# Performance work log

Measured on AMD Instinct MI355X. Metric: run time of the kernel, lower is better.

The kernel has to match this reference:

```python
import jax, jax.numpy as jnp
import numpy as np

N = 100000   # nodes
E = 1600000  # edges
EL = 200000  # decode pairs
D_IN, D_HID, D_OUT = 128, 128, 64


def setup_inputs() -> dict:
    key = jax.random.key(0)
    ks = jax.random.split(key, 9)
    x = jax.random.normal(ks[0], (N, D_IN), dtype=jnp.float32)
    edge_index = jax.random.randint(ks[1], (2, E), 0, N, dtype=jnp.int64)
    edge_label_index = jax.random.randint(ks[2], (2, EL), 0, N, dtype=jnp.int64)
    # GCNConv params: weight [in, out] (no bias inside linear), bias added after aggregation
    W1 = jax.random.normal(ks[3], (D_IN, D_HID), dtype=jnp.float32) / np.sqrt(D_IN)
    b1 = jnp.zeros((D_HID,), dtype=jnp.float32)
    W2 = jax.random.normal(ks[4], (D_HID, D_HID), dtype=jnp.float32) / np.sqrt(D_HID)
    b2 = jnp.zeros((D_HID,), dtype=jnp.float32)
    W3 = jax.random.normal(ks[5], (D_HID, D_OUT), dtype=jnp.float32) / np.sqrt(D_HID)
    b3 = jnp.zeros((D_OUT,), dtype=jnp.float32)
    return {"x": x, "edge_index": edge_index, "edge_label_index": edge_label_index,
            "W1": W1, "b1": b1, "W2": W2, "b2": b2, "W3": W3, "b3": b3}


def _gcn_norm(edge_index, num_nodes, dtype):
    # add self-loops, compute symmetric normalization deg^-1/2[src]*deg^-1/2[dst]
    loop = jnp.arange(num_nodes, dtype=edge_index.dtype)
    src = jnp.concatenate([edge_index[0], loop])
    dst = jnp.concatenate([edge_index[1], loop])
    deg = jax.ops.segment_sum(jnp.ones(src.shape, dtype=dtype), dst, num_segments=num_nodes)
    dinv = jax.lax.rsqrt(deg)  # deg >= 1 due to self-loops
    norm = dinv[src] * dinv[dst]
    return src, dst, norm


def _gcn_conv(h, W, b, src, dst, norm, num_nodes):
    h = h @ W                               # [N, out]
    msg = h[src] * norm[:, None]            # gather + scale  [E+N, out]
    out = jax.ops.segment_sum(msg, dst, num_segments=num_nodes)  # scatter-add
    return out + b


def reference(x, edge_index, edge_label_index, W1, b1, W2, b2, W3, b3):
    num_nodes = x.shape[0]
    src, dst, norm = _gcn_norm(edge_index, num_nodes, x.dtype)
    h = jax.nn.relu(_gcn_conv(x, W1, b1, src, dst, norm, num_nodes))
    h = jax.nn.relu(_gcn_conv(h, W2, b2, src, dst, norm, num_nodes))  # dropout is identity in eval
    z = _gcn_conv(h, W3, b3, src, dst, norm, num_nodes)
    # decode: dot product over candidate pairs
    return jnp.sum(z[edge_label_index[0]] * z[edge_label_index[1]], axis=-1)
```

## Files before the change

kernel.cpp:

```cpp
#include <hip/hip_runtime.h>
#include <hip/hip_bf16.h>

#define N_NODES 100000
#define N_EDGES 1600000
#define N_EL    200000

#define NB_SCAN ((N_NODES + 255) / 256)
#define CPAD 16
#define GT_GEMM ((N_NODES + 63) / 64)
#define GE_RANK ((N_EDGES + 255) / 256)

typedef unsigned int uint32;
typedef unsigned short ushort16;
typedef __attribute__((ext_vector_type(8))) short short8;
typedef __attribute__((ext_vector_type(4))) float f32x4;

static __device__ __forceinline__ ushort16 f2bf(float f) {
    uint32 u = __float_as_uint(f);
    u += 0x7fffu + ((u >> 16) & 1u);
    return (ushort16)(u >> 16);
}
static __device__ __forceinline__ float bf_lo(uint32 p) { return __uint_as_float(p << 16); }
static __device__ __forceinline__ float bf_hi(uint32 p) { return __uint_as_float(p & 0xffff0000u); }
static __device__ __forceinline__ float bf2f(ushort16 h) { return __uint_as_float((uint32)h << 16); }

__global__ void k_scan1(const int* __restrict__ cpad, int* __restrict__ rowptr,
                        int* __restrict__ bsum, float* __restrict__ dinv) {
    __shared__ int s[256];
    int t = threadIdx.x;
    int i = blockIdx.x * 256 + t;
    int v = (i < N_NODES) ? cpad[(size_t)i * CPAD] : 0;
    if (i < N_NODES) dinv[i] = 1.0f / sqrtf((float)(v + 1));
    s[t] = v;
    __syncthreads();
    for (int off = 1; off < 256; off <<= 1) {
        int u = (t >= off) ? s[t - off] : 0;
        __syncthreads();
        s[t] += u;
        __syncthreads();
    }
    if (i < N_NODES) rowptr[i] = s[t] - v;
    if (t == 255) bsum[blockIdx.x] = s[255];
}

__global__ void k_scan2(const int* __restrict__ bsum, int* __restrict__ boff) {
    __shared__ int s[512];
    int t = threadIdx.x;
    int v = (t < NB_SCAN) ? bsum[t] : 0;
    s[t] = v;
    __syncthreads();
    for (int off = 1; off < 512; off <<= 1) {
        int u = (t >= off) ? s[t - off] : 0;
        __syncthreads();
        s[t] += u;
        __syncthreads();
    }
    if (t < NB_SCAN) boff[t] = s[t] - v;
    if (t == NB_SCAN - 1) boff[NB_SCAN] = s[t];
}

__global__ void k_scan3(int* __restrict__ rowptr, const int* __restrict__ boff) {
    int i = blockIdx.x * 256 + threadIdx.x;
    if (i < N_NODES) rowptr[i] += boff[blockIdx.x];
    if (i == 0) rowptr[N_NODES] = boff[NB_SCAN];
}

__global__ void k_fill2(const int* __restrict__ src, const int* __restrict__ dst,
                        const int* __restrict__ rowptr, const int* __restrict__ r,
                        int* __restrict__ col) {
    int e = blockIdx.x * blockDim.x + threadIdx.x;
    if (e >= N_EDGES) return;
    int pos = rowptr[dst[e]] + r[e];
    __builtin_nontemporal_store(src[e], &col[pos]);
}

static __device__ __forceinline__ short8 load_afrag(const float* arow, int off) {
    float4 a0 = *(const float4*)(arow + off);
    float4 a1 = *(const float4*)(arow + off + 4);
    short8 af;
    af[0] = (short)f2bf(a0.x); af[1] = (short)f2bf(a0.y);
    af[2] = (short)f2bf(a0.z); af[3] = (short)f2bf(a0.w);
    af[4] = (short)f2bf(a1.x); af[5] = (short)f2bf(a1.y);
    af[6] = (short)f2bf(a1.z); af[7] = (short)f2bf(a1.w);
    return af;
}
static __device__ __forceinline__ short8 load_afrag(const ushort16* arow, int off) {
    return *(const short8*)(arow + off);
}

template <int D, typename AT, bool SCALE, int OS>
static __device__ __forceinline__ void gemm_body(int bid, const AT* __restrict__ A,
        const float* __restrict__ W, const float* __restrict__ dinv,
        ushort16* __restrict__ C) {
    constexpr int NT = D / 16;
    constexpr int LNT = (NT == 8) ? 3 : 2;
    __shared__ short sB[4 * NT * 64 * 8];

    int tid = threadIdx.x;

    constexpr int COMBOS = 4 * 4 * NT * 16;
    for (int cc = tid; cc < COMBOS; cc += 256) {
        int nn = cc & 15;
        int nt = (cc >> 4) & (NT - 1);
        int q  = (cc >> (4 + LNT)) & 3;
        int kt = cc >> (6 + LNT);
        short8 pk;
#pragma unroll
        for (int j = 0; j < 8; ++j)
            pk[j] = (short)f2bf(W[(kt * 32 + q * 8 + j) * D + nt * 16 + nn]);
        *(short8*)&sB[(((kt * NT + nt) * 64) + q * 16 + nn) * 8] = pk;
    }
    __syncthreads();

    int w = tid >> 6;
    int l = tid & 63;
    int q = l >> 4;
    int nn15 = l & 15;
    int m0 = bid * 64 + w * 16;

    f32x4 acc[NT];
#pragma unroll
    for (int i = 0; i < NT; ++i) acc[i] = (f32x4){0.f, 0.f, 0.f, 0.f};

    int m = m0 + nn15;
    m = min(m, N_NODES - 1);
    const AT* arow = A + (size_t)m * 128;

#pragma unroll
    for (int kt = 0; kt < 4; ++kt) {
        short8 af = load_afrag(arow, kt * 32 + q * 8);
#pragma unroll
        for (int nt = 0; nt < NT; ++nt) {
            short8 bf = *(const short8*)&sB[((kt * NT + nt) * 64 + l) * 8];
            acc[nt] = __builtin_amdgcn_mfma_f32_16x16x32_bf16(af, bf, acc[nt], 0, 0, 0);
        }
    }

    float4 dv;
    if constexpr (SCALE) dv = *(const float4*)(dinv + m0 + 4 * q);
    const float* dvp = (const float*)&dv;
#pragma unroll
    for (int nt = 0; nt < NT; ++nt) {
#pragma unroll
        for (int r = 0; r < 4; ++r) {
            int node = m0 + q * 4 + r;
            if (node < N_NODES) {
                float val = acc[nt][r];
                if constexpr (SCALE) val *= dvp[r];
                C[(size_t)node * OS + nt * 16 + nn15] = f2bf(val);
            }
        }
    }
}

template <int D, typename AT, bool SCALE, int OS>
__global__ __launch_bounds__(256, 4) void k_gemm_mfma(const AT* __restrict__ A,
        const float* __restrict__ W, const float* __restrict__ dinv,
        ushort16* __restrict__ C) {
    gemm_body<D, AT, SCALE, OS>(blockIdx.x, A, W, dinv, C);
}

__global__ __launch_bounds__(256, 4) void k_fat1(const float* __restrict__ A,
        const float* __restrict__ W, ushort16* __restrict__ C,
        const int* __restrict__ dst, int* __restrict__ cpad, int* __restrict__ r) {
    unsigned bid = blockIdx.x;
    unsigned g = bid / 5u;
    if (bid % 5u == 0u) {
        gemm_body<128, float, false, 128>(g, A, W, nullptr, C);
    } else {
        unsigned rid = g * 4u + (bid % 5u) - 1u;
        unsigned e = rid * 256u + threadIdx.x;
        if (e < N_EDGES) r[e] = atomicAdd(&cpad[(size_t)dst[e] * CPAD], 1);
    }
}

template <bool RELU, bool WEIGHTED>
__global__ void k_gather128(const int* __restrict__ rowptr, const int* __restrict__ col,
                            const float* __restrict__ dinv, const uint32* __restrict__ t,
                            const float* __restrict__ b, uint32* __restrict__ outbuf) {
    __shared__ int   sc[4][64];
    __shared__ float sd[4][64];
    int tid = threadIdx.x;
    unsigned wid = (blockIdx.x * 256u + tid) >> 6;
    if (wid >= N_NODES) return;
    int w = tid >> 6;
    int lane = tid & 63;
    int beg = rowptr[wid], end = rowptr[wid + 1];
    float di = dinv[wid];
    uint32 p = t[(size_t)wid * 64 + lane];
    float ax, ay;
    if (WEIGHTED) { ax = di * bf_lo(p); ay = di * bf_hi(p); }
    else          { ax = bf_lo(p);      ay = bf_hi(p);      }
    for (int base = beg; base < end; base += 64) {
        int cnt = min(end - base, 64);
        int c = WEIGHTED ? 0 : N_NODES;
        if (lane < cnt) c = col[base + lane];
        sc[w][lane] = c;
        if (WEIGHTED) sd[w][lane] = (lane < cnt) ? dinv[c] : 0.f;
        int nb = (cnt + 7) >> 3;
        for (int j8 = 0; j8 < nb; ++j8) {
            int j = j8 << 3;
            int s0 = sc[w][j+0], s1 = sc[w][j+1], s2 = sc[w][j+2], s3 = sc[w][j+3];
            int s4 = sc[w][j+4], s5 = sc[w][j+5], s6 = sc[w][j+6], s7 = sc[w][j+7];
            uint32 v0 = t[(size_t)s0 * 64 + lane];
            uint32 v1 = t[(size_t)s1 * 64 + lane];
            uint32 v2 = t[(size_t)s2 * 64 + lane];
            uint32 v3 = t[(size_t)s3 * 64 + lane];
            uint32 v4 = t[(size_t)s4 * 64 + lane];
            uint32 v5 = t[(size_t)s5 * 64 + lane];
            uint32 v6 = t[(size_t)s6 * 64 + lane];
            uint32 v7 = t[(size_t)s7 * 64 + lane];
            if (WEIGHTED) {
                float d0 = sd[w][j+0], d1 = sd[w][j+1], d2 = sd[w][j+2], d3 = sd[w][j+3];
                float d4 = sd[w][j+4], d5 = sd[w][j+5], d6 = sd[w][j+6], d7 = sd[w][j+7];
                ax = fmaf(d0, bf_lo(v0), ax); ay = fmaf(d0, bf_hi(v0), ay);
                ax = fmaf(d1, bf_lo(v1), ax); ay = fmaf(d1, bf_hi(v1), ay);
                ax = fmaf(d2, bf_lo(v2), ax); ay = fmaf(d2, bf_hi(v2), ay);
                ax = fmaf(d3, bf_lo(v3), ax); ay = fmaf(d3, bf_hi(v3), ay);
                ax = fmaf(d4, bf_lo(v4), ax); ay = fmaf(d4, bf_hi(v4), ay);
                ax = fmaf(d5, bf_lo(v5), ax); ay = fmaf(d5, bf_hi(v5), ay);
                ax = fmaf(d6, bf_lo(v6), ax); ay = fmaf(d6, bf_hi(v6), ay);
                ax = fmaf(d7, bf_lo(v7), ax); ay = fmaf(d7, bf_hi(v7), ay);
            } else {
                ax += (bf_lo(v0) + bf_lo(v1)) + (bf_lo(v2) + bf_lo(v3))
                    + ((bf_lo(v4) + bf_lo(v5)) + (bf_lo(v6) + bf_lo(v7)));
                ay += (bf_hi(v0) + bf_hi(v1)) + (bf_hi(v2) + bf_hi(v3))
                    + ((bf_hi(v4) + bf_hi(v5)) + (bf_hi(v6) + bf_hi(v7)));
            }
        }
    }
    float2 bb = ((const float2*)b)[lane];
    float ox = di * ax + bb.x;
    float oy = di * ay + bb.y;
    if (RELU) { ox = fmaxf(ox, 0.f); oy = fmaxf(oy, 0.f); }
    __builtin_nontemporal_store((uint32)f2bf(ox) | ((uint32)f2bf(oy) << 16),
                                &outbuf[(size_t)wid * 64 + lane]);
}

template <bool RELU>
__global__ void k_gather64(const int* __restrict__ rowptr, const int* __restrict__ col,
                           const float* __restrict__ dinv, const ushort16* __restrict__ t,
                           const float* __restrict__ b, ushort16* __restrict__ outbuf) {
    __shared__ int sc[4][64];
    int tid = threadIdx.x;
    unsigned wid = (blockIdx.x * 256u + tid) >> 6;
    if (wid >= N_NODES) return;
    int w = tid >> 6;
    int lane = tid & 63;
    int beg = rowptr[wid], end = rowptr[wid + 1];
    float di = dinv[wid];
    float acc = bf2f(t[(size_t)wid * 128 + lane]);
    for (int base = beg; base < end; base += 64) {
        int cnt = min(end - base, 64);
        int c = N_NODES;
        if (lane < cnt) c = col[base + lane];
        sc[w][lane] = c;
        int nb = (cnt + 7) >> 3;
        for (int j8 = 0; j8 < nb; ++j8) {
            int j = j8 << 3;
            int s0 = sc[w][j+0], s1 = sc[w][j+1], s2 = sc[w][j+2], s3 = sc[w][j+3];
            int s4 = sc[w][j+4], s5 = sc[w][j+5], s6 = sc[w][j+6], s7 = sc[w][j+7];
            float v0 = bf2f(t[(size_t)s0 * 128 + lane]);
            float v1 = bf2f(t[(size_t)s1 * 128 + lane]);
            float v2 = bf2f(t[(size_t)s2 * 128 + lane]);
            float v3 = bf2f(t[(size_t)s3 * 128 + lane]);
            float v4 = bf2f(t[(size_t)s4 * 128 + lane]);
            float v5 = bf2f(t[(size_t)s5 * 128 + lane]);
            float v6 = bf2f(t[(size_t)s6 * 128 + lane]);
            float v7 = bf2f(t[(size_t)s7 * 128 + lane]);
            acc += (v0 + v1) + (v2 + v3) + ((v4 + v5) + (v6 + v7));
        }
    }
    float o = di * acc + b[lane];
    if (RELU) o = fmaxf(o, 0.f);
    __builtin_nontemporal_store(f2bf(o), &outbuf[(size_t)wid * 64 + lane]);
}

__global__ void k_decode(const int* __restrict__ eli, const ushort16* __restrict__ z,
                         float* __restrict__ out) {
    int e = blockIdx.x * blockDim.x + threadIdx.x;
    if (e >= N_EL) return;
    int a = eli[e];
    int b = eli[N_EL + e];
    const uint4* za = (const uint4*)(z + (size_t)a * 64);
    const uint4* zb = (const uint4*)(z + (size_t)b * 64);
    float acc = 0.0f;
#pragma unroll
    for (int i = 0; i < 8; ++i) {
        uint4 va = za[i], vb = zb[i];
        acc += bf_lo(va.x) * bf_lo(vb.x) + bf_hi(va.x) * bf_hi(vb.x);
        acc += bf_lo(va.y) * bf_lo(vb.y) + bf_hi(va.y) * bf_hi(vb.y);
        acc += bf_lo(va.z) * bf_lo(vb.z) + bf_hi(va.z) * bf_hi(vb.z);
        acc += bf_lo(va.w) * bf_lo(vb.w) + bf_hi(va.w) * bf_hi(vb.w);
    }
    out[e] = acc;
}

extern "C" void kernel_launch(void* const* d_in, const int* in_sizes, int n_in,
                              void* d_out, int out_size, void* d_ws, size_t ws_size,
                              hipStream_t stream) {
    const float* x   = (const float*)d_in[0];
    const int*   ei  = (const int*)d_in[1];
    const int*   eli = (const int*)d_in[2];
    const float* W1  = (const float*)d_in[3];
    const float* b1  = (const float*)d_in[4];
    const float* W2  = (const float*)d_in[5];
    const float* b2  = (const float*)d_in[6];
    const float* W3  = (const float*)d_in[7];
    const float* b3  = (const float*)d_in[8];
    float* out = (float*)d_out;

    const int* srcA = ei;
    const int* dstA = ei + N_EDGES;

    char* ws = (char*)d_ws;
    float*    dinv   = (float*)   (ws + 0);
    int*      rowptr = (int*)     (ws + (1024u << 10));
    int*      bsum   = (int*)     (ws + (1888u << 10));
    int*      boff   = (int*)     (ws + (1896u << 10));
    int*      col    = (int*)     (ws + (2048u << 10));
    int*      r      = (int*)     (ws + (9u << 20));
    ushort16* t      = (ushort16*)(ws + (16u << 20));
    ushort16* aggb   = (ushort16*)(ws + (48u << 20));
    int*      cpad   = (int*)     (ws + (80u << 20));

    const int B = 256;
    const int gG  = (N_NODES * 64 + B - 1) / B;
    const int gEL = (N_EL + B - 1) / B;

    hipMemsetAsync(cpad, 0, (size_t)N_NODES * CPAD * sizeof(int), stream);
    hipMemsetAsync((char*)t + (size_t)N_NODES * 256, 0, 256, stream);
    k_fat1<<<GT_GEMM + GE_RANK, B, 0, stream>>>(x, W1, t, dstA, cpad, r);
    k_scan1<<<NB_SCAN, 256, 0, stream>>>(cpad, rowptr, bsum, dinv);
    k_scan2<<<1, 512, 0, stream>>>(bsum, boff);
    k_scan3<<<NB_SCAN, 256, 0, stream>>>(rowptr, boff);
    k_fill2<<<GE_RANK, B, 0, stream>>>(srcA, dstA, rowptr, r, col);

    k_gather128<true, true><<<gG, B, 0, stream>>>(rowptr, col, dinv, (const uint32*)t,
                                                  b1, (uint32*)aggb);
    k_gemm_mfma<128, ushort16, true, 128><<<GT_GEMM, B, 0, stream>>>(aggb, W2, dinv, t);
    k_gather128<true, false><<<gG, B, 0, stream>>>(rowptr, col, dinv, (const uint32*)t,
                                                   b2, (uint32*)aggb);
    k_gemm_mfma<64, ushort16, true, 128><<<GT_GEMM, B, 0, stream>>>(aggb, W3, dinv, t);
    k_gather64<false><<<gG, B, 0, stream>>>(rowptr, col, dinv, t, b3, aggb);

    k_decode<<<gEL, B, 0, stream>>>(eli, aggb, out);
}
```

Measured before the change: 431.1 us.

## Fuse CSR scan into single-pass kernel and prescale layer-1 features by dinv

Replaces the three-kernel scan with one kernel that computes local prefix sums and has the last-arriving block scan the block totals via an atomic counter. Consumers add a per-512-node block offset to the local row pointer, so no separate fix-up pass is needed. The CSR fill kernel now also prescales the layer-1 GEMM output by dinv, which lets the first gather use the cheaper unweighted path with no per-edge dinv loads. The fat kernel is rebalanced to 2 GEMM blocks per 8-edge-per-thread rank block, and launch bounds rise to 5 blocks per SM. The cost is an extra global read of boff in the gathers, plus a second bf16 rounding of the layer-1 features.

Measured after the change: 437.2 us. About the same (+1.4%).

```diff
diff --git a/kernel.cpp b/kernel.cpp
--- a/kernel.cpp
+++ b/kernel.cpp
@@ -5,10 +5,13 @@
 #define N_EDGES 1600000
 #define N_EL    200000
 
-#define NB_SCAN ((N_NODES + 255) / 256)
 #define CPAD 16
 #define GT_GEMM ((N_NODES + 63) / 64)
-#define GE_RANK ((N_EDGES + 255) / 256)
+#define GR_RANK 782
+#define GRID_FAT (3 * GR_RANK)
+#define NB2 ((N_NODES + 511) / 512)
+#define GF_FILL ((N_EDGES + 255) / 256)
+#define GF_PRE  ((N_NODES + 1 + 3) / 4)
 
 typedef unsigned int uint32;
 typedef unsigned short ushort16;
@@ -24,29 +27,15 @@
 static __device__ __forceinline__ float bf_hi(uint32 p) { return __uint_as_float(p & 0xffff0000u); }
 static __device__ __forceinline__ float bf2f(ushort16 h) { return __uint_as_float((uint32)h << 16); }
 
-__global__ void k_scan1(const int* __restrict__ cpad, int* __restrict__ rowptr,
-                        int* __restrict__ bsum, float* __restrict__ dinv) {
-    __shared__ int s[256];
+__global__ void k_scanF(const int* __restrict__ cpad, int* __restrict__ lrp,
+                        float* __restrict__ dinv, int* __restrict__ bsum,
+                        int* __restrict__ boff, int* __restrict__ cnt) {
+    __shared__ int s[512];
+    __shared__ int lastflag;
     int t = threadIdx.x;
-    int i = blockIdx.x * 256 + t;
+    int i = blockIdx.x * 512 + t;
     int v = (i < N_NODES) ? cpad[(size_t)i * CPAD] : 0;
     if (i < N_NODES) dinv[i] = 1.0f / sqrtf((float)(v + 1));
-    s[t] = v;
-    __syncthreads();
-    for (int off = 1; off < 256; off <<= 1) {
-        int u = (t >= off) ? s[t - off] : 0;
-        __syncthreads();
-        s[t] += u;
-        __syncthreads();
-    }
-    if (i < N_NODES) rowptr[i] = s[t] - v;
-    if (t == 255) bsum[blockIdx.x] = s[255];
-}
-
-__global__ void k_scan2(const int* __restrict__ bsum, int* __restrict__ boff) {
-    __shared__ int s[512];
-    int t = threadIdx.x;
-    int v = (t < NB_SCAN) ? bsum[t] : 0;
     s[t] = v;
     __syncthreads();
     for (int off = 1; off < 512; off <<= 1) {
@@ -55,23 +44,51 @@
         s[t] += u;
         __syncthreads();
     }
-    if (t < NB_SCAN) boff[t] = s[t] - v;
-    if (t == NB_SCAN - 1) boff[NB_SCAN] = s[t];
-}
-
-__global__ void k_scan3(int* __restrict__ rowptr, const int* __restrict__ boff) {
-    int i = blockIdx.x * 256 + threadIdx.x;
-    if (i < N_NODES) rowptr[i] += boff[blockIdx.x];
-    if (i == 0) rowptr[N_NODES] = boff[NB_SCAN];
-}
-
-__global__ void k_fill2(const int* __restrict__ src, const int* __restrict__ dst,
-                        const int* __restrict__ rowptr, const int* __restrict__ r,
-                        int* __restrict__ col) {
-    int e = blockIdx.x * blockDim.x + threadIdx.x;
-    if (e >= N_EDGES) return;
-    int pos = rowptr[dst[e]] + r[e];
-    __builtin_nontemporal_store(src[e], &col[pos]);
+    if (i <= N_NODES) lrp[i] = s[t] - v;
+    if (t == 0) {
+        __hip_atomic_store(&bsum[blockIdx.x], s[511], __ATOMIC_RELEASE,
+                           __HIP_MEMORY_SCOPE_AGENT);
+        int c = __hip_atomic_fetch_add(cnt, 1, __ATOMIC_ACQ_REL,
+                                       __HIP_MEMORY_SCOPE_AGENT);
+        lastflag = (c == NB2 - 1);
+    }
+    __syncthreads();
+    if (!lastflag) return;
+    int bv = (t < NB2) ? __hip_atomic_load(&bsum[t], __ATOMIC_ACQUIRE,
+                                           __HIP_MEMORY_SCOPE_AGENT) : 0;
+    s[t] = bv;
+    __syncthreads();
+    for (int off = 1; off < 512; off <<= 1) {
+        int u = (t >= off) ? s[t - off] : 0;
+        __syncthreads();
+        s[t] += u;
+        __syncthreads();
+    }
+    if (t < NB2) boff[t] = s[t] - bv;
+}
+
+__global__ void k_fill2p(const int* __restrict__ src, const int* __restrict__ dst,
+                         const int* __restrict__ lrp, const int* __restrict__ boff,
+                         const int* __restrict__ r, int* __restrict__ col,
+                         const float* __restrict__ dinv, uint32* __restrict__ t32) {
+    unsigned bid = blockIdx.x;
+    int tid = threadIdx.x;
+    if (bid < GF_FILL) {
+        int e = bid * 256 + tid;
+        if (e >= N_EDGES) return;
+        int dd = dst[e];
+        int pos = lrp[dd] + boff[dd >> 9] + r[e];
+        __builtin_nontemporal_store(src[e], &col[pos]);
+    } else {
+        int node = (bid - GF_FILL) * 4 + (tid >> 6);
+        int lane = tid & 63;
+        if (node > N_NODES) return;
+        float di = (node < N_NODES) ? dinv[node] : 0.f;
+        size_t idx = (size_t)node * 64 + lane;
+        uint32 p = t32[idx];
+        float lo = bf_lo(p) * di, hi = bf_hi(p) * di;
+        t32[idx] = (uint32)f2bf(lo) | ((uint32)f2bf(hi) << 16);
+    }
 }
 
 static __device__ __forceinline__ short8 load_afrag(const float* arow, int off) {
@@ -154,49 +171,64 @@
 }
 
 template <int D, typename AT, bool SCALE, int OS>
-__global__ __launch_bounds__(256, 4) void k_gemm_mfma(const AT* __restrict__ A,
+__global__ __launch_bounds__(256, 5) void k_gemm_mfma(const AT* __restrict__ A,
         const float* __restrict__ W, const float* __restrict__ dinv,
         ushort16* __restrict__ C) {
     gemm_body<D, AT, SCALE, OS>(blockIdx.x, A, W, dinv, C);
 }
 
-__global__ __launch_bounds__(256, 4) void k_fat1(const float* __restrict__ A,
+__global__ __launch_bounds__(256, 5) void k_fat1(const float* __restrict__ A,
         const float* __restrict__ W, ushort16* __restrict__ C,
         const int* __restrict__ dst, int* __restrict__ cpad, int* __restrict__ r) {
     unsigned bid = blockIdx.x;
-    unsigned g = bid / 5u;
-    if (bid % 5u == 0u) {
-        gemm_body<128, float, false, 128>(g, A, W, nullptr, C);
+    unsigned g = bid / 3u;
+    unsigned rem = bid - g * 3u;
+    if (rem < 2u) {
+        unsigned gid = g * 2u + rem;
+        if (gid < GT_GEMM)
+            gemm_body<128, float, false, 128>(gid, A, W, nullptr, C);
     } else {
-        unsigned rid = g * 4u + (bid % 5u) - 1u;
-        unsigned e = rid * 256u + threadIdx.x;
-        if (e < N_EDGES) r[e] = atomicAdd(&cpad[(size_t)dst[e] * CPAD], 1);
-    }
-}
-
-template <bool RELU, bool WEIGHTED>
-__global__ void k_gather128(const int* __restrict__ rowptr, const int* __restrict__ col,
-                            const float* __restrict__ dinv, const uint32* __restrict__ t,
-                            const float* __restrict__ b, uint32* __restrict__ outbuf) {
-    __shared__ int   sc[4][64];
-    __shared__ float sd[4][64];
+        unsigned e0 = g * 2048u + threadIdx.x;
+        int d[8], rr[8];
+#pragma unroll
+        for (int k = 0; k < 8; ++k) {
+            unsigned e = e0 + k * 256u;
+            if (e < N_EDGES) d[k] = dst[e];
+        }
+#pragma unroll
+        for (int k = 0; k < 8; ++k) {
+            unsigned e = e0 + k * 256u;
+            if (e < N_EDGES) rr[k] = atomicAdd(&cpad[(size_t)d[k] * CPAD], 1);
+        }
+#pragma unroll
+        for (int k = 0; k < 8; ++k) {
+            unsigned e = e0 + k * 256u;
+            if (e < N_EDGES) __builtin_nontemporal_store(rr[k], &r[e]);
+        }
+    }
+}
+
+template <bool RELU>
+__global__ void k_gather128(const int* __restrict__ lrp, const int* __restrict__ boff,
+                            const int* __restrict__ col, const float* __restrict__ dinv,
+                            const uint32* __restrict__ t, const float* __restrict__ b,
+                            uint32* __restrict__ outbuf) {
+    __shared__ int sc[4][64];
     int tid = threadIdx.x;
     unsigned wid = (blockIdx.x * 256u + tid) >> 6;
     if (wid >= N_NODES) return;
     int w = tid >> 6;
     int lane = tid & 63;
-    int beg = rowptr[wid], end = rowptr[wid + 1];
+    int beg = lrp[wid] + boff[wid >> 9];
+    int end = lrp[wid + 1] + boff[(wid + 1) >> 9];
     float di = dinv[wid];
     uint32 p = t[(size_t)wid * 64 + lane];
-    float ax, ay;
-    if (WEIGHTED) { ax = di * bf_lo(p); ay = di * bf_hi(p); }
-    else          { ax = bf_lo(p);      ay = bf_hi(p);      }
+    float ax = bf_lo(p), ay = bf_hi(p);
     for (int base = beg; base < end; base += 64) {
         int cnt = min(end - base, 64);
-        int c = WEIGHTED ? 0 : N_NODES;
+        int c = N_NODES;
         if (lane < cnt) c = col[base + lane];
         sc[w][lane] = c;
-        if (WEIGHTED) sd[w][lane] = (lane < cnt) ? dinv[c] : 0.f;
         int nb = (cnt + 7) >> 3;
         for (int j8 = 0; j8 < nb; ++j8) {
             int j = j8 << 3;
@@ -210,23 +242,10 @@
             uint32 v5 = t[(size_t)s5 * 64 + lane];
             uint32 v6 = t[(size_t)s6 * 64 + lane];
             uint32 v7 = t[(size_t)s7 * 64 + lane];
-            if (WEIGHTED) {
-                float d0 = sd[w][j+0], d1 = sd[w][j+1], d2 = sd[w][j+2], d3 = sd[w][j+3];
-                float d4 = sd[w][j+4], d5 = sd[w][j+5], d6 = sd[w][j+6], d7 = sd[w][j+7];
-                ax = fmaf(d0, bf_lo(v0), ax); ay = fmaf(d0, bf_hi(v0), ay);
-                ax = fmaf(d1, bf_lo(v1), ax); ay = fmaf(d1, bf_hi(v1), ay);
-                ax = fmaf(d2, bf_lo(v2), ax); ay = fmaf(d2, bf_hi(v2), ay);
-                ax = fmaf(d3, bf_lo(v3), ax); ay = fmaf(d3, bf_hi(v3), ay);
-                ax = fmaf(d4, bf_lo(v4), ax); ay = fmaf(d4, bf_hi(v4), ay);
-                ax = fmaf(d5, bf_lo(v5), ax); ay = fmaf(d5, bf_hi(v5), ay);
-                ax = fmaf(d6, bf_lo(v6), ax); ay = fmaf(d6, bf_hi(v6), ay);
-                ax = fmaf(d7, bf_lo(v7), ax); ay = fmaf(d7, bf_hi(v7), ay);
-            } else {
-                ax += (bf_lo(v0) + bf_lo(v1)) + (bf_lo(v2) + bf_lo(v3))
-                    + ((bf_lo(v4) + bf_lo(v5)) + (bf_lo(v6) + bf_lo(v7)));
-                ay += (bf_hi(v0) + bf_hi(v1)) + (bf_hi(v2) + bf_hi(v3))
-                    + ((bf_hi(v4) + bf_hi(v5)) + (bf_hi(v6) + bf_hi(v7)));
-            }
+            ax += (bf_lo(v0) + bf_lo(v1)) + (bf_lo(v2) + bf_lo(v3))
+                + ((bf_lo(v4) + bf_lo(v5)) + (bf_lo(v6) + bf_lo(v7)));
+            ay += (bf_hi(v0) + bf_hi(v1)) + (bf_hi(v2) + bf_hi(v3))
+                + ((bf_hi(v4) + bf_hi(v5)) + (bf_hi(v6) + bf_hi(v7)));
         }
     }
     float2 bb = ((const float2*)b)[lane];
@@ -238,16 +257,18 @@
 }
 
 template <bool RELU>
-__global__ void k_gather64(const int* __restrict__ rowptr, const int* __restrict__ col,
-                           const float* __restrict__ dinv, const ushort16* __restrict__ t,
-                           const float* __restrict__ b, ushort16* __restrict__ outbuf) {
+__global__ void k_gather64(const int* __restrict__ lrp, const int* __restrict__ boff,
+                           const int* __restrict__ col, const float* __restrict__ dinv,
+                           const ushort16* __restrict__ t, const float* __restrict__ b,
+                           ushort16* __restrict__ outbuf) {
     __shared__ int sc[4][64];
     int tid = threadIdx.x;
     unsigned wid = (blockIdx.x * 256u + tid) >> 6;
     if (wid >= N_NODES) return;
     int w = tid >> 6;
     int lane = tid & 63;
-    int beg = rowptr[wid], end = rowptr[wid + 1];
+    int beg = lrp[wid] + boff[wid >> 9];
+    int end = lrp[wid + 1] + boff[(wid + 1) >> 9];
     float di = dinv[wid];
     float acc = bf2f(t[(size_t)wid * 128 + lane]);
     for (int base = beg; base < end; base += 64) {
@@ -315,7 +336,7 @@
 
     char* ws = (char*)d_ws;
     float*    dinv   = (float*)   (ws + 0);
-    int*      rowptr = (int*)     (ws + (1024u << 10));
+    int*      lrp    = (int*)     (ws + (1024u << 10));
     int*      bsum   = (int*)     (ws + (1888u << 10));
     int*      boff   = (int*)     (ws + (1896u << 10));
     int*      col    = (int*)     (ws + (2048u << 10));
@@ -323,26 +344,25 @@
     ushort16* t      = (ushort16*)(ws + (16u << 20));
     ushort16* aggb   = (ushort16*)(ws + (48u << 20));
     int*      cpad   = (int*)     (ws + (80u << 20));
+    int*      cnt    = cpad + (size_t)N_NODES * CPAD;
 
     const int B = 256;
     const int gG  = (N_NODES * 64 + B - 1) / B;
     const int gEL = (N_EL + B - 1) / B;
 
-    hipMemsetAsync(cpad, 0, (size_t)N_NODES * CPAD * sizeof(int), stream);
-    hipMemsetAsync((char*)t + (size_t)N_NODES * 256, 0, 256, stream);
-    k_fat1<<<GT_GEMM + GE_RANK, B, 0, stream>>>(x, W1, t, dstA, cpad, r);
-    k_scan1<<<NB_SCAN, 256, 0, stream>>>(cpad, rowptr, bsum, dinv);
-    k_scan2<<<1, 512, 0, stream>>>(bsum, boff);
-    k_scan3<<<NB_SCAN, 256, 0, stream>>>(rowptr, boff);
-    k_fill2<<<GE_RANK, B, 0, stream>>>(srcA, dstA, rowptr, r, col);
-
-    k_gather128<true, true><<<gG, B, 0, stream>>>(rowptr, col, dinv, (const uint32*)t,
-                                                  b1, (uint32*)aggb);
+    hipMemsetAsync(cpad, 0, ((size_t)N_NODES * CPAD + 16) * sizeof(int), stream);
+    k_fat1<<<GRID_FAT, B, 0, stream>>>(x, W1, t, dstA, cpad, r);
+    k_scanF<<<NB2, 512, 0, stream>>>(cpad, lrp, dinv, bsum, boff, cnt);
+    k_fill2p<<<GF_FILL + GF_PRE, B, 0, stream>>>(srcA, dstA, lrp, boff, r, col,
+                                                 dinv, (uint32*)t);
+
+    k_gather128<true><<<gG, B, 0, stream>>>(lrp, boff, col, dinv, (const uint32*)t,
+                                            b1, (uint32*)aggb);
     k_gemm_mfma<128, ushort16, true, 128><<<GT_GEMM, B, 0, stream>>>(aggb, W2, dinv, t);
-    k_gather128<true, false><<<gG, B, 0, stream>>>(rowptr, col, dinv, (const uint32*)t,
-                                                   b2, (uint32*)aggb);
+    k_gather128<true><<<gG, B, 0, stream>>>(lrp, boff, col, dinv, (const uint32*)t,
+                                            b2, (uint32*)aggb);
     k_gemm_mfma<64, ushort16, true, 128><<<GT_GEMM, B, 0, stream>>>(aggb, W3, dinv, t);
-    k_gather64<false><<<gG, B, 0, stream>>>(rowptr, col, dinv, t, b3, aggb);
+    k_gather64<false><<<gG, B, 0, stream>>>(lrp, boff, col, dinv, t, b3, aggb);
 
     k_decode<<<gEL, B, 0, stream>>>(eli, aggb, out);
 }
```
